# Kernel tuning notes

Hardware: AMD Instinct MI355X
Metric: run time of the kernel (lower is better)

The kernel has to match this reference:

```python
import jax, jax.numpy as jnp
import numpy as np

N = 262144      # total tokens
LM1 = 6         # max digit chars after the first character
D = 128         # embedding_dim
NUM_LAB = 1000
V1 = 2 * 26 + NUM_LAB  # first-level table rows (1052)


def setup_inputs() -> dict:
    key = jax.random.key(0)
    k1, k2, k3, k4, k5, k6, k7 = jax.random.split(key, 7)
    return {
        "first_chars": jax.random.randint(k1, (N,), 0, 26, dtype=jnp.int32),
        "digits": jax.random.randint(k2, (N, LM1), 0, 10, dtype=jnp.int32),
        "ndigits": jax.random.randint(k3, (N,), 0, 7, dtype=jnp.int32),
        "mods": jax.random.randint(k4, (N,), 0, 3, dtype=jnp.int32),  # 0=icd10,1=atc,2=lab
        "vals": jax.random.normal(k5, (N,), dtype=jnp.float32),
        "E1": jax.random.normal(k6, (V1, D), dtype=jnp.float32),
        "Eint": jax.random.normal(k7, (10, D), dtype=jnp.float32),
        "kappa": 2,
    }


def reference(first_chars, digits, ndigits, mods, vals, E1, Eint, kappa):
    # first-level index per modality: icd -> c+5, atc -> 2c+5, lab -> 52+code
    first_idx = jnp.where(
        mods == 0, first_chars + 5,
        jnp.where(mods == 1, first_chars * 2 + 5, 52 + first_chars))
    base = E1[first_idx]                                  # [N, D]

    # position-decayed digit accumulation: sum_i 1/(i+2)^kappa * Eint[digit_i]
    pos = jnp.arange(LM1, dtype=jnp.float32)
    w = 1.0 / (pos + 2.0) ** kappa                        # [LM1]
    mask = (jnp.arange(LM1)[None, :] < ndigits[:, None]).astype(base.dtype)
    onehot = jax.nn.one_hot(digits, 10, dtype=base.dtype)  # [N, LM1, 10]
    digit_emb = jnp.einsum("nl,nlk,kd->nd", w[None, :] * mask, onehot, Eint)

    # modality scatter: lab tokens use base * val, icd/atc use base + decayed digits
    final = jnp.where((mods == 2)[:, None], base * vals[:, None], base + digit_emb)
    return final
```

## Files before the change

### kernel.cpp

```cpp
#include <hip/hip_runtime.h>
#include <hip/hip_bf16.h>


#define LM1 6
#define D   128
#define TPB 32
#define TPT 4

__global__ __launch_bounds__(256) void hier_emb_kernel(
    const int*   __restrict__ first_chars,
    const int*   __restrict__ digits,
    const int*   __restrict__ ndigits,
    const int*   __restrict__ mods,
    const float* __restrict__ vals,
    const float* __restrict__ E1,
    const float* __restrict__ Eint,
    const int*   __restrict__ kappa_p,
    float*       __restrict__ out,
    int n)
{
    __shared__ float sEint[10][D];
    __shared__ int   sFidx[TPB];
    __shared__ int   sNd[TPB];
    __shared__ int   sMod[TPB];
    __shared__ float sVal[TPB];
    __shared__ int   sDig[TPB * LM1];

    const int tid  = threadIdx.x;
    const int tok0 = blockIdx.x * TPB;

    {
        const float4* src = reinterpret_cast<const float4*>(Eint);
        float4*       dst = reinterpret_cast<float4*>(&sEint[0][0]);
        dst[tid] = src[tid];
        const int i2 = 256 + tid;
        if (i2 < (10 * D) / 4) dst[i2] = src[i2];
    }

    if (tid < TPB) {
        int tt = tok0 + tid; if (tt >= n) tt = n - 1;
        const int mod = mods[tt];
        const int fc  = first_chars[tt];
        sMod[tid]  = mod;
        sFidx[tid] = (mod == 0) ? (fc + 5) : (mod == 1) ? (fc * 2 + 5) : (52 + fc);
        sNd[tid]   = ndigits[tt];
        sVal[tid]  = vals[tt];
    } else if (tid >= 64) {
        const int i = tid - 64;
        long gi = (long)tok0 * LM1 + i;
        const long lim = (long)n * LM1;
        if (gi >= lim) gi = lim - 1;
        sDig[i] = digits[gi];
    }

    const int k = *kappa_p;
    float w[LM1];
#pragma unroll
    for (int i = 0; i < LM1; ++i) {
        float p = 1.0f;
        const float b = (float)(i + 2);
        for (int j = 0; j < k; ++j) p *= b;
        w[i] = 1.0f / p;
    }

    __syncthreads();

    const int q   = tid & 31;
    const int ltb = (tid >> 5) * TPT;

    float4 base[TPT];
#pragma unroll
    for (int j = 0; j < TPT; ++j) {
        const int fidx = sFidx[ltb + j];
        base[j] = *reinterpret_cast<const float4*>(E1 + (size_t)fidx * D + q * 4);
    }

    float4 acc[TPT];
#pragma unroll
    for (int j = 0; j < TPT; ++j) {
        const int lt  = ltb + j;
        const int mod = sMod[lt];
        if (mod == 2) {
            const float v = sVal[lt];
            acc[j].x = base[j].x * v; acc[j].y = base[j].y * v;
            acc[j].z = base[j].z * v; acc[j].w = base[j].w * v;
        } else {
            acc[j] = base[j];
            const int nd = sNd[lt];
#pragma unroll
            for (int i = 0; i < LM1; ++i) {
                if (i < nd) {
                    const int dg = sDig[lt * LM1 + i];
                    const float4 e =
                        *reinterpret_cast<const float4*>(&sEint[dg][q * 4]);
                    acc[j].x += w[i] * e.x; acc[j].y += w[i] * e.y;
                    acc[j].z += w[i] * e.z; acc[j].w += w[i] * e.w;
                }
            }
        }
    }

#pragma unroll
    for (int j = 0; j < TPT; ++j) {
        const int tok = tok0 + ltb + j;
        if (tok < n) {
            *reinterpret_cast<float4*>(out + (size_t)tok * D + q * 4) = acc[j];
        }
    }
}

extern "C" void kernel_launch(void* const* d_in, const int* in_sizes, int n_in,
                              void* d_out, int out_size, void* d_ws, size_t ws_size,
                              hipStream_t stream) {
    const int*   first_chars = (const int*)  d_in[0];
    const int*   digits      = (const int*)  d_in[1];
    const int*   ndigits     = (const int*)  d_in[2];
    const int*   mods        = (const int*)  d_in[3];
    const float* vals        = (const float*)d_in[4];
    const float* E1          = (const float*)d_in[5];
    const float* Eint        = (const float*)d_in[6];
    const int*   kappa       = (const int*)  d_in[7];
    float*       out         = (float*)d_out;

    const int n    = in_sizes[0];
    const int grid = (n + TPB - 1) / TPB;

    hier_emb_kernel<<<grid, 256, 0, stream>>>(
        first_chars, digits, ndigits, mods, vals, E1, Eint, kappa, out, n);
}
```

Before: 166.5 us.

## Process 128 tokens per block and stream output with nontemporal stores

Each block now covers 128 tokens instead of 32, looping over four 32-token chunks. This spreads the shared-memory staging of the digit table and the block launch cost over more work. Output writes use nontemporal stores so the large write stream bypasses cache retention, and the math is rewritten with native vector types. In exchange there are four times fewer blocks, which lowers the parallelism available to hide latency.

```diff
diff --git a/kernel.cpp b/kernel.cpp
--- a/kernel.cpp
+++ b/kernel.cpp
@@ -4,8 +4,11 @@
 
 #define LM1 6
 #define D   128
-#define TPB 32
+#define TPB 128
 #define TPT 4
+#define NCHUNK (TPB / 32)
+
+typedef float nfloat4 __attribute__((ext_vector_type(4)));
 
 __global__ __launch_bounds__(256) void hier_emb_kernel(
     const int*   __restrict__ first_chars,
@@ -30,8 +33,8 @@
     const int tok0 = blockIdx.x * TPB;
 
     {
-        const float4* src = reinterpret_cast<const float4*>(Eint);
-        float4*       dst = reinterpret_cast<float4*>(&sEint[0][0]);
+        const nfloat4* src = reinterpret_cast<const nfloat4*>(Eint);
+        nfloat4*       dst = reinterpret_cast<nfloat4*>(&sEint[0][0]);
         dst[tid] = src[tid];
         const int i2 = 256 + tid;
         if (i2 < (10 * D) / 4) dst[i2] = src[i2];
@@ -45,12 +48,16 @@
         sFidx[tid] = (mod == 0) ? (fc + 5) : (mod == 1) ? (fc * 2 + 5) : (52 + fc);
         sNd[tid]   = ndigits[tt];
         sVal[tid]  = vals[tt];
-    } else if (tid >= 64) {
-        const int i = tid - 64;
-        long gi = (long)tok0 * LM1 + i;
+    }
+    {
         const long lim = (long)n * LM1;
-        if (gi >= lim) gi = lim - 1;
-        sDig[i] = digits[gi];
+#pragma unroll
+        for (int r = 0; r < (TPB * LM1) / 256; ++r) {
+            const int i = tid + r * 256;
+            long gi = (long)tok0 * LM1 + i;
+            if (gi >= lim) gi = lim - 1;
+            sDig[i] = digits[gi];
+        }
     }
 
     const int k = *kappa_p;
@@ -65,46 +72,50 @@
 
     __syncthreads();
 
-    const int q   = tid & 31;
-    const int ltb = (tid >> 5) * TPT;
+    const int q  = tid & 31;
+    const int g  = tid >> 5;
 
-    float4 base[TPT];
+#pragma unroll 2
+    for (int c = 0; c < NCHUNK; ++c) {
+        const int ltb = c * 32 + g * TPT;
+
+        nfloat4 base[TPT];
 #pragma unroll
-    for (int j = 0; j < TPT; ++j) {
-        const int fidx = sFidx[ltb + j];
-        base[j] = *reinterpret_cast<const float4*>(E1 + (size_t)fidx * D + q * 4);
-    }
+        for (int j = 0; j < TPT; ++j) {
+            const int fidx = sFidx[ltb + j];
+            base[j] = *reinterpret_cast<const nfloat4*>(E1 + (size_t)fidx * D + q * 4);
+        }
 
-    float4 acc[TPT];
+        nfloat4 acc[TPT];
 #pragma unroll
-    for (int j = 0; j < TPT; ++j) {
-        const int lt  = ltb + j;
-        const int mod = sMod[lt];
-        if (mod == 2) {
-            const float v = sVal[lt];
-            acc[j].x = base[j].x * v; acc[j].y = base[j].y * v;
-            acc[j].z = base[j].z * v; acc[j].w = base[j].w * v;
-        } else {
-            acc[j] = base[j];
-            const int nd = sNd[lt];
+        for (int j = 0; j < TPT; ++j) {
+            const int lt  = ltb + j;
+            const int mod = sMod[lt];
+            if (mod == 2) {
+                acc[j] = base[j] * sVal[lt];
+            } else {
+                acc[j] = base[j];
+                const int nd = sNd[lt];
 #pragma unroll
-            for (int i = 0; i < LM1; ++i) {
-                if (i < nd) {
-                    const int dg = sDig[lt * LM1 + i];
-                    const float4 e =
-                        *reinterpret_cast<const float4*>(&sEint[dg][q * 4]);
-                    acc[j].x += w[i] * e.x; acc[j].y += w[i] * e.y;
-                    acc[j].z += w[i] * e.z; acc[j].w += w[i] * e.w;
+                for (int i = 0; i < LM1; ++i) {
+                    if (i < nd) {
+                        const int dg = sDig[lt * LM1 + i];
+                        const nfloat4 e =
+                            *reinterpret_cast<const nfloat4*>(&sEint[dg][q * 4]);
+                        acc[j] += w[i] * e;
+                    }
                 }
             }
         }
-    }
 
 #pragma unroll
-    for (int j = 0; j < TPT; ++j) {
-        const int tok = tok0 + ltb + j;
-        if (tok < n) {
-            *reinterpret_cast<float4*>(out + (size_t)tok * D + q * 4) = acc[j];
+        for (int j = 0; j < TPT; ++j) {
+            const int tok = tok0 + ltb + j;
+            if (tok < n) {
+                __builtin_nontemporal_store(
+                    acc[j],
+                    reinterpret_cast<nfloat4*>(out + (size_t)tok * D + q * 4));
+            }
         }
     }
 }
```

Result: no change. 165.4 us (-0.7%).
